# Kernel optimization log

Measured on AMD Instinct MI355X. Metric: run time of the kernel, lower is better.

## Reference

```python
import jax, jax.numpy as jnp
import numpy as np

N, C_IN, C_OUT = 8192, 256, 128


def setup_inputs() -> dict:
    key = jax.random.key(0)
    k1, k2, k3, k4, k5 = jax.random.split(key, 5)
    features = jax.random.normal(k1, (N, C_IN), dtype=jnp.float32)
    wavelets = jax.random.normal(k2, (N, N), dtype=jnp.float32) / np.sqrt(N)
    wavelets_inv = jax.random.normal(k3, (N, N), dtype=jnp.float32) / np.sqrt(N)
    # xavier_uniform for weight_matrix
    limit = np.sqrt(6.0 / (C_IN + C_OUT))
    weight_matrix = jax.random.uniform(k4, (C_IN, C_OUT), dtype=jnp.float32, minval=-limit, maxval=limit)
    # filter init uniform(0.9, 1.1)
    filt = jax.random.uniform(k5, (N,), dtype=jnp.float32, minval=0.9, maxval=1.1)
    return {"features": features, "wavelets": wavelets, "wavelets_inv": wavelets_inv,
            "weight_matrix": weight_matrix, "filt": filt}


def reference(features, wavelets, wavelets_inv, weight_matrix, filt):
    # transformed = features @ W                         [N, C_out]
    transformed = jnp.matmul(features, weight_matrix)
    # right = wavelets_inv @ transformed                 [N, C_out]
    right = jnp.matmul(wavelets_inv, transformed)
    # wavelets @ diag(filt) == column-wise scale of wavelets by filt
    # (same math as torch.mm(wavelets, torch.diag(filter)) without the O(N^3) GEMM)
    scaled_right = right * filt[:, None]                 # equivalent: (wavelets * filt) @ right
    out = jnp.matmul(wavelets, scaled_right)             # [N, C_out]
    return out
```

## Files before the change

kernel.cpp:

```cpp
#include <hip/hip_runtime.h>

#define MROWS 8192
#define NCOLS 128
#define LDT 88
#define KSTEP 64
#define SPLITK 8

using f32x4  = __attribute__((ext_vector_type(4))) float;
using bf16x8 = __attribute__((ext_vector_type(8))) short;
using u32x4  = __attribute__((ext_vector_type(4))) unsigned int;
using u32x2  = __attribute__((ext_vector_type(2))) unsigned int;

__device__ __forceinline__ unsigned short f2bf(float f) {
    unsigned int u = __float_as_uint(f);
    u += 0x7fffu + ((u >> 16) & 1u);
    return (unsigned short)(u >> 16);
}
__device__ __forceinline__ unsigned int pk2(float a, float b) {
    return (unsigned int)f2bf(a) | ((unsigned int)f2bf(b) << 16);
}

template <int OUTMODE>
__global__ __launch_bounds__(256, 2) void gemm_kernel(
    const float* __restrict__ A,
    const unsigned short* __restrict__ Bt,
    void* __restrict__ out,
    int Kdim, int KC, int ldb)
{
    __shared__ __align__(16) unsigned short As[128 * LDT];
    __shared__ __align__(16) unsigned short Bs[128 * LDT];

    const int tid  = threadIdx.x;
    const int wave = tid >> 6;
    const int lane = tid & 63;
    const int lrow = lane & 15;
    const int lq   = lane >> 4;
    const int mq   = (wave & 1) * 64;
    const int nq   = (wave >> 1) * 64;
    const int m0   = blockIdx.x * 128;
    const int s    = blockIdx.y;
    const int kbase = s * KC;
    const int iters = KC >> 6;

    const int trow = tid >> 3;
    const int tk   = (tid & 7) * 8;

    f32x4 areg[4][2];
    u32x4 breg[4];

    const float*          Aptr = A  + (size_t)(m0 + trow) * Kdim + tk;
    const unsigned short* Bptr = Bt + (size_t)trow * ldb + tk;

    auto load_stage = [&](int k0) {
#pragma unroll
        for (int p = 0; p < 4; ++p) {
            const float* ap = Aptr + (size_t)(p * 32) * Kdim + k0;
            areg[p][0] = *(const f32x4*)(ap);
            areg[p][1] = *(const f32x4*)(ap + 4);
            breg[p]    = *(const u32x4*)(Bptr + (size_t)(p * 32) * ldb + k0);
        }
    };
    auto store_stage = [&]() {
#pragma unroll
        for (int p = 0; p < 4; ++p) {
            int row = trow + p * 32;
            u32x4 av;
            av.x = pk2(areg[p][0].x, areg[p][0].y);
            av.y = pk2(areg[p][0].z, areg[p][0].w);
            av.z = pk2(areg[p][1].x, areg[p][1].y);
            av.w = pk2(areg[p][1].z, areg[p][1].w);
            *(u32x4*)&As[row * LDT + tk] = av;
            *(u32x4*)&Bs[row * LDT + tk] = breg[p];
        }
    };

    f32x4 acc[4][4];
#pragma unroll
    for (int i = 0; i < 4; ++i)
#pragma unroll
        for (int j = 0; j < 4; ++j)
            acc[i][j] = {0.f, 0.f, 0.f, 0.f};

    load_stage(kbase);
    for (int it = 0; it < iters; ++it) {
        __syncthreads();
        store_stage();
        __syncthreads();
        if (it + 1 < iters) load_stage(kbase + (it + 1) * KSTEP);
#pragma unroll
        for (int kk = 0; kk < 2; ++kk) {
            const int ko = kk * 32 + lq * 8;
            bf16x8 afr[4], bfr[4];
#pragma unroll
            for (int mt = 0; mt < 4; ++mt)
                afr[mt] = *(bf16x8*)&As[(mq + mt * 16 + lrow) * LDT + ko];
#pragma unroll
            for (int nt = 0; nt < 4; ++nt)
                bfr[nt] = *(bf16x8*)&Bs[(nq + nt * 16 + lrow) * LDT + ko];
#pragma unroll
            for (int mt = 0; mt < 4; ++mt)
#pragma unroll
                for (int nt = 0; nt < 4; ++nt)
                    acc[mt][nt] = __builtin_amdgcn_mfma_f32_16x16x32_bf16(
                        afr[mt], bfr[nt], acc[mt][nt], 0, 0, 0);
        }
    }

    if (OUTMODE == 0) {
        float* P = (float*)out + (size_t)s * (MROWS * NCOLS);
#pragma unroll
        for (int mt = 0; mt < 4; ++mt) {
            int r = m0 + mq + mt * 16 + lq * 4;
#pragma unroll
            for (int nt = 0; nt < 4; ++nt) {
                int c = nq + nt * 16 + lrow;
                *(f32x4*)&P[(size_t)c * MROWS + r] = acc[mt][nt];
            }
        }
    } else if (OUTMODE == 1) {
        float* P = (float*)out + (size_t)s * (MROWS * NCOLS);
#pragma unroll
        for (int mt = 0; mt < 4; ++mt) {
            int r = m0 + mq + mt * 16 + lq * 4;
#pragma unroll
            for (int nt = 0; nt < 4; ++nt) {
                int c = nq + nt * 16 + lrow;
#pragma unroll
                for (int e = 0; e < 4; ++e)
                    P[(size_t)(r + e) * NCOLS + c] = acc[mt][nt][e];
            }
        }
    } else {
        unsigned short* Tt = (unsigned short*)out;
#pragma unroll
        for (int mt = 0; mt < 4; ++mt) {
            int r = m0 + mq + mt * 16 + lq * 4;
#pragma unroll
            for (int nt = 0; nt < 4; ++nt) {
                int c = nq + nt * 16 + lrow;
                u32x2 v;
                v.x = pk2(acc[mt][nt][0], acc[mt][nt][1]);
                v.y = pk2(acc[mt][nt][2], acc[mt][nt][3]);
                *(u32x2*)&Tt[(size_t)c * MROWS + r] = v;
            }
        }
    }
}

__global__ void convert_w(const float* __restrict__ W, unsigned short* __restrict__ Wt) {
    int idx = blockIdx.x * 256 + threadIdx.x;
    int k = idx >> 7, c = idx & 127;
    Wt[c * 256 + k] = f2bf(W[idx]);
}

__global__ void reduce2(const float* __restrict__ P, const float* __restrict__ filt,
                        unsigned short* __restrict__ Rt) {
    int idx4 = (blockIdx.x * 256 + threadIdx.x) * 4;
    f32x4 sum = {0.f, 0.f, 0.f, 0.f};
#pragma unroll
    for (int s = 0; s < SPLITK; ++s)
        sum += *(const f32x4*)&P[(size_t)s * (MROWS * NCOLS) + idx4];
    int r = idx4 & (MROWS - 1);
    f32x4 fl = *(const f32x4*)&filt[r];
    sum *= fl;
    u32x2 v;
    v.x = pk2(sum.x, sum.y);
    v.y = pk2(sum.z, sum.w);
    *(u32x2*)&Rt[idx4] = v;
}

__global__ void reduce3(const float* __restrict__ P, float* __restrict__ outp) {
    int idx4 = (blockIdx.x * 256 + threadIdx.x) * 4;
    f32x4 sum = {0.f, 0.f, 0.f, 0.f};
#pragma unroll
    for (int s = 0; s < SPLITK; ++s)
        sum += *(const f32x4*)&P[(size_t)s * (MROWS * NCOLS) + idx4];
    *(f32x4*)&outp[idx4] = sum;
}

extern "C" void kernel_launch(void* const* d_in, const int* in_sizes, int n_in,
                              void* d_out, int out_size, void* d_ws, size_t ws_size,
                              hipStream_t stream) {
    const float* features     = (const float*)d_in[0];
    const float* wavelets     = (const float*)d_in[1];
    const float* wavelets_inv = (const float*)d_in[2];
    const float* W            = (const float*)d_in[3];
    const float* filt         = (const float*)d_in[4];
    float* outp = (float*)d_out;

    char* ws = (char*)d_ws;
    float*          P  = (float*)ws;
    unsigned short* Tt = (unsigned short*)(ws + (size_t)32 * 1024 * 1024);
    unsigned short* Rt = (unsigned short*)(ws + (size_t)34 * 1024 * 1024);
    unsigned short* Wt = (unsigned short*)(ws + (size_t)36 * 1024 * 1024);

    convert_w<<<128, 256, 0, stream>>>(W, Wt);
    gemm_kernel<2><<<dim3(64, 1), 256, 0, stream>>>(features, Wt, (void*)Tt, 256, 256, 256);
    gemm_kernel<0><<<dim3(64, 8), 256, 0, stream>>>(wavelets_inv, Tt, (void*)P, 8192, 1024, 8192);
    reduce2<<<1024, 256, 0, stream>>>(P, filt, Rt);
    gemm_kernel<1><<<dim3(64, 8), 256, 0, stream>>>(wavelets, Rt, (void*)P, 8192, 1024, 8192);
    reduce3<<<1024, 256, 0, stream>>>(P, outp);
}
```

Baseline: 627.2 us.

## Load MFMA fragments directly from global memory, bypassing LDS staging

Replaces the shared-memory tiled GEMM with a version where each lane loads its A and B MFMA fragments directly from global memory into registers. It double-buffers them across 32-wide k steps and converts A to bf16 in registers. This removes LDS stores/loads and the two barriers per k-step. In exchange, A rows are fetched redundantly by the two waves sharing the same row block, and global access patterns become less coalesced.

```diff
diff --git a/kernel.cpp b/kernel.cpp
--- a/kernel.cpp
+++ b/kernel.cpp
@@ -2,8 +2,6 @@
 
 #define MROWS 8192
 #define NCOLS 128
-#define LDT 88
-#define KSTEP 64
 #define SPLITK 8
 
 using f32x4  = __attribute__((ext_vector_type(4))) float;
@@ -21,15 +19,12 @@
 }
 
 template <int OUTMODE>
-__global__ __launch_bounds__(256, 2) void gemm_kernel(
+__global__ __launch_bounds__(256, 2) void gemm_direct(
     const float* __restrict__ A,
     const unsigned short* __restrict__ Bt,
     void* __restrict__ out,
     int Kdim, int KC, int ldb)
 {
-    __shared__ __align__(16) unsigned short As[128 * LDT];
-    __shared__ __align__(16) unsigned short Bs[128 * LDT];
-
     const int tid  = threadIdx.x;
     const int wave = tid >> 6;
     const int lane = tid & 63;
@@ -40,39 +35,15 @@
     const int m0   = blockIdx.x * 128;
     const int s    = blockIdx.y;
     const int kbase = s * KC;
-    const int iters = KC >> 6;
 
-    const int trow = tid >> 3;
-    const int tk   = (tid & 7) * 8;
-
-    f32x4 areg[4][2];
-    u32x4 breg[4];
-
-    const float*          Aptr = A  + (size_t)(m0 + trow) * Kdim + tk;
-    const unsigned short* Bptr = Bt + (size_t)trow * ldb + tk;
-
-    auto load_stage = [&](int k0) {
+    const float*          Arow[4];
+    const unsigned short* Brow[4];
 #pragma unroll
-        for (int p = 0; p < 4; ++p) {
-            const float* ap = Aptr + (size_t)(p * 32) * Kdim + k0;
-            areg[p][0] = *(const f32x4*)(ap);
-            areg[p][1] = *(const f32x4*)(ap + 4);
-            breg[p]    = *(const u32x4*)(Bptr + (size_t)(p * 32) * ldb + k0);
-        }
-    };
-    auto store_stage = [&]() {
+    for (int mt = 0; mt < 4; ++mt)
+        Arow[mt] = A + (size_t)(m0 + mq + mt * 16 + lrow) * Kdim + kbase + lq * 8;
 #pragma unroll
-        for (int p = 0; p < 4; ++p) {
-            int row = trow + p * 32;
-            u32x4 av;
-            av.x = pk2(areg[p][0].x, areg[p][0].y);
-            av.y = pk2(areg[p][0].z, areg[p][0].w);
-            av.z = pk2(areg[p][1].x, areg[p][1].y);
-            av.w = pk2(areg[p][1].z, areg[p][1].w);
-            *(u32x4*)&As[row * LDT + tk] = av;
-            *(u32x4*)&Bs[row * LDT + tk] = breg[p];
-        }
-    };
+    for (int nt = 0; nt < 4; ++nt)
+        Brow[nt] = Bt + (size_t)(nq + nt * 16 + lrow) * ldb + kbase + lq * 8;
 
     f32x4 acc[4][4];
 #pragma unroll
@@ -81,29 +52,44 @@
         for (int j = 0; j < 4; ++j)
             acc[i][j] = {0.f, 0.f, 0.f, 0.f};
 
-    load_stage(kbase);
-    for (int it = 0; it < iters; ++it) {
-        __syncthreads();
-        store_stage();
-        __syncthreads();
-        if (it + 1 < iters) load_stage(kbase + (it + 1) * KSTEP);
+    f32x4 a0[2][4], a1[2][4];
+    u32x4 bv[2][4];
+
+    auto load_frag = [&](int buf, int k) {
 #pragma unroll
-        for (int kk = 0; kk < 2; ++kk) {
-            const int ko = kk * 32 + lq * 8;
-            bf16x8 afr[4], bfr[4];
+        for (int mt = 0; mt < 4; ++mt) {
+            a0[buf][mt] = *(const f32x4*)(Arow[mt] + k);
+            a1[buf][mt] = *(const f32x4*)(Arow[mt] + k + 4);
+        }
 #pragma unroll
-            for (int mt = 0; mt < 4; ++mt)
-                afr[mt] = *(bf16x8*)&As[(mq + mt * 16 + lrow) * LDT + ko];
+        for (int nt = 0; nt < 4; ++nt)
+            bv[buf][nt] = *(const u32x4*)(Brow[nt] + k);
+    };
+
+    load_frag(0, 0);
+    int cur = 0;
+    for (int k = 0; k < KC; k += 32) {
+        const int kn = (k + 32 < KC) ? k + 32 : k;
+        load_frag(cur ^ 1, kn);
+
+        bf16x8 af[4], bf[4];
+#pragma unroll
+        for (int mt = 0; mt < 4; ++mt) {
+            u32x4 av;
+            av.x = pk2(a0[cur][mt].x, a0[cur][mt].y);
+            av.y = pk2(a0[cur][mt].z, a0[cur][mt].w);
+            av.z = pk2(a1[cur][mt].x, a1[cur][mt].y);
+            av.w = pk2(a1[cur][mt].z, a1[cur][mt].w);
+            af[mt] = __builtin_bit_cast(bf16x8, av);
+            bf[mt] = __builtin_bit_cast(bf16x8, bv[cur][mt]);
+        }
+#pragma unroll
+        for (int mt = 0; mt < 4; ++mt)
 #pragma unroll
             for (int nt = 0; nt < 4; ++nt)
-                bfr[nt] = *(bf16x8*)&Bs[(nq + nt * 16 + lrow) * LDT + ko];
-#pragma unroll
-            for (int mt = 0; mt < 4; ++mt)
-#pragma unroll
-                for (int nt = 0; nt < 4; ++nt)
-                    acc[mt][nt] = __builtin_amdgcn_mfma_f32_16x16x32_bf16(
-                        afr[mt], bfr[nt], acc[mt][nt], 0, 0, 0);
-        }
+                acc[mt][nt] = __builtin_amdgcn_mfma_f32_16x16x32_bf16(
+                    af[mt], bf[nt], acc[mt][nt], 0, 0, 0);
+        cur ^= 1;
     }
 
     if (OUTMODE == 0) {
@@ -195,9 +181,9 @@
     unsigned short* Wt = (unsigned short*)(ws + (size_t)36 * 1024 * 1024);
 
     convert_w<<<128, 256, 0, stream>>>(W, Wt);
-    gemm_kernel<2><<<dim3(64, 1), 256, 0, stream>>>(features, Wt, (void*)Tt, 256, 256, 256);
-    gemm_kernel<0><<<dim3(64, 8), 256, 0, stream>>>(wavelets_inv, Tt, (void*)P, 8192, 1024, 8192);
+    gemm_direct<2><<<dim3(64, 1), 256, 0, stream>>>(features, Wt, (void*)Tt, 256, 256, 256);
+    gemm_direct<0><<<dim3(64, 8), 256, 0, stream>>>(wavelets_inv, Tt, (void*)P, 8192, 1024, 8192);
     reduce2<<<1024, 256, 0, stream>>>(P, filt, Rt);
-    gemm_kernel<1><<<dim3(64, 8), 256, 0, stream>>>(wavelets, Rt, (void*)P, 8192, 1024, 8192);
+    gemm_direct<1><<<dim3(64, 8), 256, 0, stream>>>(wavelets, Rt, (void*)P, 8192, 1024, 8192);
     reduce3<<<1024, 256, 0, stream>>>(P, outp);
 }
```

After: 870.9 us. +38.9%, slower.
